# Kernel tuning notes

Measured on AMD Instinct MI355X. Metric: run time of the kernel, lower is better.

The kernel has to match this reference:

```python
import jax, jax.numpy as jnp
import numpy as np

EPS = 1e-5  # BatchNorm1d default eps


def gcn_conv(x, src, dst, w, b, n):
    # src/dst already include self-loops. Symmetric normalization D^-1/2 (A+I) D^-1/2.
    deg = jnp.zeros((n,), x.dtype).at[dst].add(1.0)
    dinv = jnp.where(deg > 0, jax.lax.rsqrt(jnp.maximum(deg, 1.0)), 0.0)
    norm = dinv[src] * dinv[dst]                      # [E+N]
    h = x @ w                                          # [B, N, H]
    msg = h[:, src, :] * norm[None, :, None]           # gather + scale  [B, E+N, H]
    agg = jnp.zeros_like(h).at[:, dst, :].add(msg)     # scatter-add
    return agg + b


def batch_norm(h, gamma, beta):
    # training-mode BN over the flattened (B*N) axis, biased variance (torch BN forward)
    mu = h.mean(axis=(0, 1))
    var = ((h - mu) ** 2).mean(axis=(0, 1))
    return (h - mu) * jax.lax.rsqrt(var + EPS) * gamma + beta


def reference(x, edge_index, W1, b1, W2, b2, gamma1, beta1, gamma2, beta2, Wc, bc):
    n = x.shape[1]
    loops = jnp.arange(n)
    src = jnp.concatenate([edge_index[0], loops])
    dst = jnp.concatenate([edge_index[1], loops])
    h = jax.nn.relu(gcn_conv(x, src, dst, W1, b1, n))
    h = batch_norm(h, gamma1, beta1)
    # dropout(p=0.2) treated as identity (eval / deterministic reference)
    h = jax.nn.relu(gcn_conv(h, src, dst, W2, b2, n))
    h = batch_norm(h, gamma2, beta2)
    out = (h @ Wc + bc).squeeze(-1)                    # [B, N]
    return out


def setup_inputs() -> dict:
    key = jax.random.key(0)
    ks = jax.random.split(key, 8)
    B, N, E, F, H = 4, 20000, 320000, 64, 128
    s = lambda fan: 1.0 / np.sqrt(fan)
    return {
        "x": jax.random.normal(ks[0], (B, N, F), dtype=jnp.float32),
        "edge_index": jax.random.randint(ks[1], (2, E), 0, N, dtype=jnp.int64),
        "W1": jax.random.normal(ks[2], (F, H), dtype=jnp.float32) * s(F),
        "b1": jnp.zeros((H,), jnp.float32),
        "W2": jax.random.normal(ks[3], (H, H), dtype=jnp.float32) * s(H),
        "b2": jnp.zeros((H,), jnp.float32),
        "gamma1": jnp.ones((H,), jnp.float32),
        "beta1": jnp.zeros((H,), jnp.float32),
        "gamma2": jnp.ones((H,), jnp.float32),
        "beta2": jnp.zeros((H,), jnp.float32),
        "Wc": jax.random.normal(ks[4], (H, 1), dtype=jnp.float32) * s(H),
        "bc": jnp.zeros((1,), jnp.float32),
    }
```

## Files before the change

kernel.cpp:

```cpp
#include <hip/hip_runtime.h>

constexpr int Bb = 4;
constexpr int Nn = 20000;
constexpr int Ff = 64;
constexpr int Hh = 128;
constexpr float BN_EPS = 1e-5f;
constexpr int NSLOTS = 64;
constexpr int NB = (Nn + 1023) / 1024;

typedef __attribute__((ext_vector_type(8))) short bf16x8;
typedef __attribute__((ext_vector_type(4))) float f32x4;

__device__ inline unsigned f2bf(float f) {
    unsigned u = __float_as_uint(f);
    return (u + 0x7fffu + ((u >> 16) & 1u)) >> 16;
}
__device__ inline unsigned pack2(float lo, float hi) { return f2bf(lo) | (f2bf(hi) << 16); }
__device__ inline float bf_lo(unsigned w) { return __uint_as_float(w << 16); }
__device__ inline float bf_hi(unsigned w) { return __uint_as_float(w & 0xffff0000u); }

template <int NU>
__device__ inline void ldrow(unsigned* u, const unsigned* p) {
    if constexpr (NU == 2) { const uint2 t = *(const uint2*)p; u[0] = t.x; u[1] = t.y; }
    else { const uint4 t = *(const uint4*)p; u[0] = t.x; u[1] = t.y; u[2] = t.z; u[3] = t.w; }
}
template <int NU>
__device__ inline void acc_row(float* a, const unsigned* u, float nm) {
#pragma unroll
    for (int c = 0; c < NU; ++c) {
        a[2 * c]     = fmaf(nm, bf_lo(u[c]), a[2 * c]);
        a[2 * c + 1] = fmaf(nm, bf_hi(u[c]), a[2 * c + 1]);
    }
}

__global__ void k_deg(const int* __restrict__ dst, int E, int* __restrict__ deg) {
    int e = blockIdx.x * blockDim.x + threadIdx.x;
    if (e < E) atomicAdd(&deg[dst[e]], 1);
}

__global__ __launch_bounds__(1024) void k_scan1(const int* __restrict__ deg,
                                                int* __restrict__ rowptr,
                                                int* __restrict__ bsum) {
    __shared__ int wsum[16];
    const int tid = threadIdx.x, lane = tid & 63, wid = tid >> 6;
    const int i = blockIdx.x * 1024 + tid;
    const int cnt = (i < Nn) ? (deg[i] + 1) : 0;
    int v = cnt;
#pragma unroll
    for (int d = 1; d < 64; d <<= 1) {
        const int t = __shfl_up(v, d);
        if (lane >= d) v += t;
    }
    if (lane == 63) wsum[wid] = v;
    __syncthreads();
    if (wid == 0) {
        const int orig = (lane < 16) ? wsum[lane] : 0;
        int w = orig;
#pragma unroll
        for (int d = 1; d < 16; d <<= 1) {
            const int t = __shfl_up(w, d);
            if (lane >= d) w += t;
        }
        if (lane == 15) bsum[blockIdx.x] = w;
        if (lane < 16) wsum[lane] = w - orig;
    }
    __syncthreads();
    if (i < Nn) rowptr[i] = wsum[wid] + (v - cnt);
}

__global__ void k_scan2(int* __restrict__ bsum) {
    const int lane = threadIdx.x;
    const int v = (lane < NB) ? bsum[lane] : 0;
    int s = v;
#pragma unroll
    for (int d = 1; d < 64; d <<= 1) {
        const int t = __shfl_up(s, d);
        if (lane >= d) s += t;
    }
    if (lane < NB) bsum[lane] = s - v;
}

__global__ __launch_bounds__(1024) void k_scan3(const int* __restrict__ deg,
                                                int* __restrict__ rowptr,
                                                const int* __restrict__ bsum,
                                                int* __restrict__ cursor,
                                                float* __restrict__ dinv) {
    const int i = blockIdx.x * 1024 + threadIdx.x;
    if (i >= Nn) return;
    const int cnt = deg[i] + 1;
    const int excl = rowptr[i] + bsum[blockIdx.x];
    rowptr[i] = excl;
    cursor[i] = excl;
    dinv[i] = rsqrtf((float)cnt);
    if (i == Nn - 1) rowptr[Nn] = excl + cnt;
}

__global__ void k_fill(const int* __restrict__ src, const int* __restrict__ dst, int E,
                       const float* __restrict__ dinv, int* __restrict__ cursor,
                       int* __restrict__ csr_src, float* __restrict__ csr_norm,
                       float* __restrict__ nsum) {
    int t = blockIdx.x * blockDim.x + threadIdx.x;
    int s, d;
    if (t < E) { s = src[t]; d = dst[t]; }
    else if (t < E + Nn) { s = d = t - E; }
    else return;
    int pos = atomicAdd(&cursor[d], 1);
    const float nm = dinv[s] * dinv[d];
    csr_src[pos]  = s;
    csr_norm[pos] = nm;
    atomicAdd(&nsum[d], nm);
}

__global__ void k_cvt(const float* __restrict__ x, unsigned* __restrict__ xb) {
    const int t = blockIdx.x * 256 + threadIdx.x;
    if (t >= Bb * Nn * 32) return;
    const int c2 = t & 31;
    const int bn = t >> 5;
    const int n  = bn % Nn;
    const int b  = bn / Nn;
    const float2 v = *(const float2*)&x[(size_t)t * 2];
    xb[((size_t)n * Bb + b) * 32 + c2] = pack2(v.x, v.y);
}

__global__ void k_wt1(const float* __restrict__ W, unsigned short* __restrict__ WTf) {
    const int f = blockIdx.x * 256 + threadIdx.x;
    if (f >= 128 * Ff) return;
    const int j = f & 7, lane = (f >> 3) & 63, rest = f >> 9;
    const int ks = rest & 1, tt = rest >> 1;
    const int col = tt * 16 + (lane & 15);
    const int k = ks * 32 + ((lane >> 4) << 3) + j;
    WTf[f] = (unsigned short)f2bf(W[(size_t)k * 128 + col]);
}

__global__ __launch_bounds__(128) void k_prep2(const float* __restrict__ gsum,
                                               const float* __restrict__ gsq,
                                               const float* __restrict__ gamma,
                                               const float* __restrict__ beta,
                                               const float* __restrict__ W2,
                                               unsigned short* __restrict__ WT2f,
                                               float* __restrict__ shW2) {
    __shared__ float sc_s[128], sh_s[128];
    const int c = threadIdx.x;
    float s = 0.f, q = 0.f;
    for (int j = 0; j < NSLOTS; ++j) { s += gsum[j * 128 + c]; q += gsq[j * 128 + c]; }
    const float inv = 1.0f / (float)(Bb * Nn);
    const float mu  = s * inv;
    const float var = q * inv - mu * mu;
    const float sc  = gamma[c] * rsqrtf(var + BN_EPS);
    sc_s[c] = sc;
    sh_s[c] = beta[c] - mu * sc;
    __syncthreads();
    if (blockIdx.x < 64) {
#pragma unroll
        for (int i = 0; i < 2; ++i) {
            const int f = blockIdx.x * 256 + i * 128 + c;
            const int j = f & 7, lane = (f >> 3) & 63, rest = f >> 9;
            const int ks = rest & 3, tt = rest >> 2;
            const int col = tt * 16 + (lane & 15);
            const int k = ks * 32 + ((lane >> 4) << 3) + j;
            WT2f[f] = (unsigned short)f2bf(sc_s[k] * W2[(size_t)k * 128 + col]);
        }
    } else {
        float a = 0.f;
        for (int k = 0; k < 128; ++k) a = fmaf(sh_s[k], W2[(size_t)k * 128 + c], a);
        shW2[c] = a;
    }
}

template <int K, bool L2E>
__global__ __launch_bounds__(256, 4) void k_fmm(const unsigned* __restrict__ G,
                                                const int* __restrict__ rowptr,
                                                const int* __restrict__ csr_src,
                                                const float* __restrict__ csr_norm,
                                                const unsigned short* __restrict__ WTf,
                                                const float* __restrict__ bias,
                                                const float* __restrict__ nsum,
                                                const float* __restrict__ shW2,
                                                unsigned short* __restrict__ Yout,
                                                float* __restrict__ gsum,
                                                float* __restrict__ gsq) {
    constexpr int NKS = K / 32;
    constexpr int AST = K + 8;
    constexpr int NU = K / 32;
    constexpr int ROWU = Bb * K / 2;
    __shared__ alignas(16) unsigned short sA[64 * AST];
    __shared__ float lsum[128], lsq[128];

    const int tid = threadIdx.x;
    const int w = tid >> 6, lane = tid & 63;
    const int cg = lane & 15, kg = lane >> 4;
    const int row0 = blockIdx.x * 64;
    if (tid < 128) { lsum[tid] = 0.f; lsq[tid] = 0.f; }
    __syncthreads();

#pragma unroll
    for (int j = 0; j < 4; ++j) {
        const int nl = w * 4 + j;
        const int v = blockIdx.x * 16 + nl;
        const int beg = rowptr[v], end = rowptr[v + 1];
        float a[2 * NU];
#pragma unroll
        for (int c = 0; c < 2 * NU; ++c) a[c] = 0.f;
        int e = beg;
        for (; e + 8 <= end; e += 8) {
            unsigned u[8][NU];
            int si[8];
#pragma unroll
            for (int q = 0; q < 8; ++q) si[q] = csr_src[e + q];
#pragma unroll
            for (int q = 0; q < 8; ++q)
                ldrow<NU>(u[q], G + (size_t)si[q] * ROWU + lane * NU);
#pragma unroll
            for (int q = 0; q < 8; ++q) acc_row<NU>(a, u[q], csr_norm[e + q]);
        }
        for (; e + 4 <= end; e += 4) {
            unsigned u[4][NU];
            int si[4];
#pragma unroll
            for (int q = 0; q < 4; ++q) si[q] = csr_src[e + q];
#pragma unroll
            for (int q = 0; q < 4; ++q)
                ldrow<NU>(u[q], G + (size_t)si[q] * ROWU + lane * NU);
#pragma unroll
            for (int q = 0; q < 4; ++q) acc_row<NU>(a, u[q], csr_norm[e + q]);
        }
        for (; e < end; ++e) {
            unsigned u[NU];
            ldrow<NU>(u, G + (size_t)csr_src[e] * ROWU + lane * NU);
            acc_row<NU>(a, u, csr_norm[e]);
        }
        const int row = nl * 4 + kg;
        unsigned p[NU];
#pragma unroll
        for (int c = 0; c < NU; ++c) p[c] = pack2(a[2 * c], a[2 * c + 1]);
        if constexpr (NU == 2) *(uint2*)&sA[row * AST + cg * 4] = *(const uint2*)p;
        else                   *(uint4*)&sA[row * AST + cg * 8] = *(const uint4*)p;
    }

    const int rowL = w * 16 + cg;
    f32x4 acc[8];
#pragma unroll
    for (int t = 0; t < 8; ++t) acc[t] = (f32x4){0.f, 0.f, 0.f, 0.f};
#pragma unroll
    for (int ks = 0; ks < NKS; ++ks) {
        const bf16x8 av = *(const bf16x8*)&sA[rowL * AST + ks * 32 + kg * 8];
#pragma unroll
        for (int t = 0; t < 8; ++t) {
            const bf16x8 bv = *(const bf16x8*)&WTf[(size_t)((t * NKS + ks) * 64 + lane) * 8];
            acc[t] = __builtin_amdgcn_mfma_f32_16x16x32_bf16(av, bv, acc[t], 0, 0, 0);
        }
    }

    const int rbase = w * 16 + kg * 4;
    float ns = 0.f;
    if (L2E) ns = nsum[(row0 + rbase) >> 2];
#pragma unroll
    for (int t = 0; t < 8; ++t) {
        const int col = t * 16 + cg;
        float badd = bias[col];
        if (L2E) badd = fmaf(ns, shW2[col], badd);
        float s = 0.f, q = 0.f;
#pragma unroll
        for (int jj = 0; jj < 4; ++jj) {
            const float y = fmaxf(acc[t][jj] + badd, 0.f);
            Yout[(size_t)(row0 + rbase + jj) * 128 + col] = (unsigned short)f2bf(y);
            s += y; q = fmaf(y, y, q);
        }
        atomicAdd(&lsum[col], s);
        atomicAdd(&lsq[col], q);
    }
    __syncthreads();
    float* gs = gsum + (size_t)(blockIdx.x & (NSLOTS - 1)) * 128;
    float* gq = gsq  + (size_t)(blockIdx.x & (NSLOTS - 1)) * 128;
    if (tid < 128) { atomicAdd(&gs[tid], lsum[tid]); atomicAdd(&gq[tid], lsq[tid]); }
}

__global__ void k_bnfin2(const float* __restrict__ gsum, const float* __restrict__ gsq,
                         const float* __restrict__ gamma, const float* __restrict__ beta,
                         const float* __restrict__ Wc, const float* __restrict__ bc,
                         float* __restrict__ wcs, float* __restrict__ kc) {
    __shared__ float red[128];
    const int c = threadIdx.x;
    float s = 0.f, q = 0.f;
    for (int j = 0; j < NSLOTS; ++j) { s += gsum[j * 128 + c]; q += gsq[j * 128 + c]; }
    const float inv = 1.0f / (float)(Bb * Nn);
    const float mu  = s * inv;
    const float var = q * inv - mu * mu;
    const float sc  = gamma[c] * rsqrtf(var + BN_EPS);
    const float sh  = beta[c] - mu * sc;
    const float w   = Wc[c];
    wcs[c] = sc * w;
    red[c] = sh * w;
    __syncthreads();
    for (int st = 64; st; st >>= 1) {
        if (c < st) red[c] += red[c + st];
        __syncthreads();
    }
    if (c == 0) kc[0] = red[0] + bc[0];
}

__global__ __launch_bounds__(256) void k_cls(const unsigned* __restrict__ h2,
                                             const float* __restrict__ wcs,
                                             const float* __restrict__ kc,
                                             float* __restrict__ out) {
    const int wave = threadIdx.x >> 6;
    const int lane = threadIdx.x & 63;
    const size_t row = (size_t)blockIdx.x * 4 + wave;
    if (row >= (size_t)Bb * Nn) return;
    const unsigned w = h2[row * 64 + lane];
    const float2 wc = *(const float2*)&wcs[lane * 2];
    float p = bf_lo(w) * wc.x + bf_hi(w) * wc.y;
#pragma unroll
    for (int off = 32; off; off >>= 1) p += __shfl_down(p, off);
    if (lane == 0) {
        const int n = (int)(row >> 2), b = (int)(row & 3);
        out[(size_t)b * Nn + n] = p + kc[0];
    }
}

extern "C" void kernel_launch(void* const* d_in, const int* in_sizes, int n_in,
                              void* d_out, int out_size, void* d_ws, size_t ws_size,
                              hipStream_t stream) {
    const float* x      = (const float*)d_in[0];
    const int*   ei     = (const int*)d_in[1];
    const float* W1     = (const float*)d_in[2];
    const float* b1     = (const float*)d_in[3];
    const float* W2     = (const float*)d_in[4];
    const float* b2     = (const float*)d_in[5];
    const float* gamma1 = (const float*)d_in[6];
    const float* beta1  = (const float*)d_in[7];
    const float* gamma2 = (const float*)d_in[8];
    const float* beta2  = (const float*)d_in[9];
    const float* Wc     = (const float*)d_in[10];
    const float* bc     = (const float*)d_in[11];
    float* out = (float*)d_out;

    const int E = in_sizes[1] / 2;
    const int* src = ei;
    const int* dst = ei + E;

    char* ws = (char*)d_ws;
    size_t off = 0;
    auto alloc = [&](size_t bytes) -> char* {
        char* p = ws + off;
        off += (bytes + 255) & ~(size_t)255;
        return p;
    };
    int*      deg      = (int*)     alloc((size_t)Nn * 4);
    float*    nsum     = (float*)   alloc((size_t)Nn * 4);
    float*    gstat    = (float*)   alloc((size_t)4 * NSLOTS * 128 * 4);
    const size_t zspan = (size_t)((char*)(gstat + 4 * NSLOTS * 128) - (char*)deg);
    float* gsum1 = gstat;
    float* gsq1  = gstat + NSLOTS * 128;
    float* gsum2 = gstat + 2 * NSLOTS * 128;
    float* gsq2  = gstat + 3 * NSLOTS * 128;

    int*      cursor   = (int*)     alloc((size_t)Nn * 4);
    int*      rowptr   = (int*)     alloc((size_t)(Nn + 1) * 4);
    int*      bsum     = (int*)     alloc((size_t)NB * 4);
    float*    dinv     = (float*)   alloc((size_t)Nn * 4);
    int*      csr_src  = (int*)     alloc((size_t)(E + Nn) * 4);
    float*    csr_norm = (float*)   alloc((size_t)(E + Nn) * 4);
    float*    wcs      = (float*)   alloc(128 * 4);
    float*    kc       = (float*)   alloc(256);
    unsigned short* WT1f = (unsigned short*)alloc((size_t)128 * Ff * 2);
    unsigned short* WT2f = (unsigned short*)alloc((size_t)128 * Hh * 2);
    float*          shW2 = (float*)         alloc((size_t)128 * 4);
    unsigned*       xb   = (unsigned*)      alloc((size_t)Nn * Bb * 32 * 4);
    unsigned short* h1b  = (unsigned short*)alloc((size_t)Bb * Nn * Hh * 2);
    unsigned short* h2b  = (unsigned short*)alloc((size_t)Bb * Nn * Hh * 2);

    (void)hipMemsetAsync(deg, 0, zspan, stream);

    k_deg<<<(E + 255) / 256, 256, 0, stream>>>(dst, E, deg);
    k_scan1<<<NB, 1024, 0, stream>>>(deg, rowptr, bsum);
    k_scan2<<<1, 64, 0, stream>>>(bsum);
    k_scan3<<<NB, 1024, 0, stream>>>(deg, rowptr, bsum, cursor, dinv);
    k_fill<<<(E + Nn + 255) / 256, 256, 0, stream>>>(src, dst, E, dinv, cursor,
                                                     csr_src, csr_norm, nsum);
    k_cvt<<<(Bb * Nn * 32 + 255) / 256, 256, 0, stream>>>(x, xb);
    k_wt1<<<(128 * Ff) / 256, 256, 0, stream>>>(W1, WT1f);

    k_fmm<Ff, false><<<Nn / 16, 256, 0, stream>>>(
        xb, rowptr, csr_src, csr_norm, WT1f, b1, nullptr, nullptr, h1b, gsum1, gsq1);
    k_prep2<<<65, 128, 0, stream>>>(gsum1, gsq1, gamma1, beta1, W2, WT2f, shW2);
    k_fmm<Hh, true><<<Nn / 16, 256, 0, stream>>>(
        (const unsigned*)h1b, rowptr, csr_src, csr_norm, WT2f, b2, nsum, shW2,
        h2b, gsum2, gsq2);
    k_bnfin2<<<1, Hh, 0, stream>>>(gsum2, gsq2, gamma2, beta2, Wc, bc, wcs, kc);

    k_cls<<<(Bb * Nn + 3) / 4, 256, 0, stream>>>((const unsigned*)h2b, wcs, kc, out);
}
```

Measured before the change: 223.0 us.

## Run fused aggregate-matmul kernel as single-wave blocks with shuffle-reduced BN stats

Turns the fused gather-aggregate + MFMA kernel from 256-thread blocks (four waves, 16 nodes) into 64-thread single-wave blocks handling 4 nodes each, with a smaller LDS tile and no block barriers. The per-block LDS atomic reduction of BatchNorm sums is replaced by wave shuffles followed by direct global atomics into the slot arrays. This is meant to cut barrier stalls and tail imbalance from uneven node degrees. In exchange it issues four times as many blocks and many more global atomics on the 64 statistic slots, which may add contention.

```diff
diff --git a/kernel.cpp b/kernel.cpp
--- a/kernel.cpp
+++ b/kernel.cpp
@@ -168,35 +168,31 @@
 }
 
 template <int K, bool L2E>
-__global__ __launch_bounds__(256, 4) void k_fmm(const unsigned* __restrict__ G,
-                                                const int* __restrict__ rowptr,
-                                                const int* __restrict__ csr_src,
-                                                const float* __restrict__ csr_norm,
-                                                const unsigned short* __restrict__ WTf,
-                                                const float* __restrict__ bias,
-                                                const float* __restrict__ nsum,
-                                                const float* __restrict__ shW2,
-                                                unsigned short* __restrict__ Yout,
-                                                float* __restrict__ gsum,
-                                                float* __restrict__ gsq) {
+__global__ __launch_bounds__(64, 6) void k_fmm(const unsigned* __restrict__ G,
+                                               const int* __restrict__ rowptr,
+                                               const int* __restrict__ csr_src,
+                                               const float* __restrict__ csr_norm,
+                                               const unsigned short* __restrict__ WTf,
+                                               const float* __restrict__ bias,
+                                               const float* __restrict__ nsum,
+                                               const float* __restrict__ shW2,
+                                               unsigned short* __restrict__ Yout,
+                                               float* __restrict__ gsum,
+                                               float* __restrict__ gsq) {
     constexpr int NKS = K / 32;
     constexpr int AST = K + 8;
     constexpr int NU = K / 32;
     constexpr int ROWU = Bb * K / 2;
-    __shared__ alignas(16) unsigned short sA[64 * AST];
-    __shared__ float lsum[128], lsq[128];
-
-    const int tid = threadIdx.x;
-    const int w = tid >> 6, lane = tid & 63;
+    __shared__ alignas(16) unsigned short sA[16 * AST];
+
+    const int lane = threadIdx.x;
     const int cg = lane & 15, kg = lane >> 4;
-    const int row0 = blockIdx.x * 64;
-    if (tid < 128) { lsum[tid] = 0.f; lsq[tid] = 0.f; }
-    __syncthreads();
+    const int g = blockIdx.x;
+    const int row0 = g * 16;
 
 #pragma unroll
     for (int j = 0; j < 4; ++j) {
-        const int nl = w * 4 + j;
-        const int v = blockIdx.x * 16 + nl;
+        const int v = g * 4 + j;
         const int beg = rowptr[v], end = rowptr[v + 1];
         float a[2 * NU];
 #pragma unroll
@@ -229,7 +225,7 @@
             ldrow<NU>(u, G + (size_t)csr_src[e] * ROWU + lane * NU);
             acc_row<NU>(a, u, csr_norm[e]);
         }
-        const int row = nl * 4 + kg;
+        const int row = j * 4 + kg;
         unsigned p[NU];
 #pragma unroll
         for (int c = 0; c < NU; ++c) p[c] = pack2(a[2 * c], a[2 * c + 1]);
@@ -237,13 +233,12 @@
         else                   *(uint4*)&sA[row * AST + cg * 8] = *(const uint4*)p;
     }
 
-    const int rowL = w * 16 + cg;
     f32x4 acc[8];
 #pragma unroll
     for (int t = 0; t < 8; ++t) acc[t] = (f32x4){0.f, 0.f, 0.f, 0.f};
 #pragma unroll
     for (int ks = 0; ks < NKS; ++ks) {
-        const bf16x8 av = *(const bf16x8*)&sA[rowL * AST + ks * 32 + kg * 8];
+        const bf16x8 av = *(const bf16x8*)&sA[cg * AST + ks * 32 + kg * 8];
 #pragma unroll
         for (int t = 0; t < 8; ++t) {
             const bf16x8 bv = *(const bf16x8*)&WTf[(size_t)((t * NKS + ks) * 64 + lane) * 8];
@@ -251,9 +246,11 @@
         }
     }
 
-    const int rbase = w * 16 + kg * 4;
+    const int rbase = kg * 4;
     float ns = 0.f;
-    if (L2E) ns = nsum[(row0 + rbase) >> 2];
+    if (L2E) ns = nsum[g * 4 + kg];
+    float* gs = gsum + (size_t)(g & (NSLOTS - 1)) * 128;
+    float* gq = gsq  + (size_t)(g & (NSLOTS - 1)) * 128;
 #pragma unroll
     for (int t = 0; t < 8; ++t) {
         const int col = t * 16 + cg;
@@ -266,13 +263,10 @@
             Yout[(size_t)(row0 + rbase + jj) * 128 + col] = (unsigned short)f2bf(y);
             s += y; q = fmaf(y, y, q);
         }
-        atomicAdd(&lsum[col], s);
-        atomicAdd(&lsq[col], q);
-    }
-    __syncthreads();
-    float* gs = gsum + (size_t)(blockIdx.x & (NSLOTS - 1)) * 128;
-    float* gq = gsq  + (size_t)(blockIdx.x & (NSLOTS - 1)) * 128;
-    if (tid < 128) { atomicAdd(&gs[tid], lsum[tid]); atomicAdd(&gq[tid], lsq[tid]); }
+        s += __shfl_xor(s, 16); s += __shfl_xor(s, 32);
+        q += __shfl_xor(q, 16); q += __shfl_xor(q, 32);
+        if (kg == 0) { atomicAdd(&gs[col], s); atomicAdd(&gq[col], q); }
+    }
 }
 
 __global__ void k_bnfin2(const float* __restrict__ gsum, const float* __restrict__ gsq,
@@ -381,10 +375,10 @@
     k_cvt<<<(Bb * Nn * 32 + 255) / 256, 256, 0, stream>>>(x, xb);
     k_wt1<<<(128 * Ff) / 256, 256, 0, stream>>>(W1, WT1f);
 
-    k_fmm<Ff, false><<<Nn / 16, 256, 0, stream>>>(
+    k_fmm<Ff, false><<<Nn / 4, 64, 0, stream>>>(
         xb, rowptr, csr_src, csr_norm, WT1f, b1, nullptr, nullptr, h1b, gsum1, gsq1);
     k_prep2<<<65, 128, 0, stream>>>(gsum1, gsq1, gamma1, beta1, W2, WT2f, shW2);
-    k_fmm<Hh, true><<<Nn / 16, 256, 0, stream>>>(
+    k_fmm<Hh, true><<<Nn / 4, 64, 0, stream>>>(
         (const unsigned*)h1b, rowptr, csr_src, csr_norm, WT2f, b2, nsum, shW2,
         h2b, gsum2, gsq2);
     k_bnfin2<<<1, Hh, 0, stream>>>(gsum2, gsq2, gamma2, beta2, Wc, bc, wcs, kc);
```

Measured after the change: 184.2 us. -17.4%, faster.
